# Kernel optimization log

Hardware: AMD Instinct MI355X
Metric: run time of the kernel (lower is better)

## Reference

```python
import jax, jax.numpy as jnp
import numpy as np

B, T, D_MODEL, N_HEAD = 8, 1024, 1024, 8
D_K = D_MODEL // N_HEAD  # = d_v = 128; V projection shared across heads


def setup_inputs() -> dict:
    key = jax.random.key(0)
    ks = jax.random.split(key, 8)
    scale = 0.02
    q = jax.random.normal(ks[0], (B, T, D_MODEL), jnp.float32)
    k = jax.random.normal(ks[1], (B, T, D_MODEL), jnp.float32)
    v = jax.random.normal(ks[2], (B, T, D_MODEL), jnp.float32)
    # causal mask, 1.0 = attend, broadcast to batch (shape (B, T, T))
    mask = jnp.broadcast_to(jnp.tril(jnp.ones((T, T), jnp.float32)), (B, T, T))
    Wq = jax.random.normal(ks[3], (N_HEAD, D_MODEL, D_K), jnp.float32) * scale
    Wk = jax.random.normal(ks[4], (N_HEAD, D_MODEL, D_K), jnp.float32) * scale
    Wv = jax.random.normal(ks[5], (D_MODEL, D_K), jnp.float32) * scale  # shared across heads
    Wo = jax.random.normal(ks[6], (D_K, D_MODEL), jnp.float32) * scale
    return {"q": q, "k": k, "v": v, "mask": mask, "Wq": Wq, "Wk": Wk, "Wv": Wv, "Wo": Wo}


def reference(q, k, v, mask, Wq, Wk, Wv, Wo):
    # Per-head Q/K projections (batched over heads), shared V projection.
    qh = jnp.einsum('btd,hdk->hbtk', q, Wq)  # (H,B,T,d_k)
    kh = jnp.einsum('bsd,hdk->hbsk', k, Wk)  # (H,B,S,d_k)
    vh = jnp.einsum('bsd,dk->bsk', v, Wv)    # (B,S,d_v) shared across heads
    temper = jnp.sqrt(jnp.asarray(qh.shape[-1], jnp.float32))
    scores = jnp.einsum('hbtk,hbsk->hbts', qh, kh) / temper
    scores = scores + (-1e9) * (1.0 - mask)[None]  # additive mask per head
    attn = jax.nn.softmax(scores, axis=-1)          # (H,B,T,S)
    heads = jnp.einsum('hbts,bsk->hbtk', attn, vh)  # (H,B,T,d_v)
    out = jnp.einsum('btk,kd->btd', heads.mean(axis=0), Wo)  # mean over heads, then w_o
    return out, attn  # dropout rate 0.0 / inference -> identity
```

## Files before the change

kernel.cpp:

```cpp
#include <hip/hip_runtime.h>
#include <cstdint>

typedef __attribute__((ext_vector_type(8))) short bf16x8;
typedef __attribute__((ext_vector_type(4))) float f32x4;

constexpr int NH = 8, NB = 8, SEQ = 1024, DM = 1024, DK = 128;
constexpr int MTOT = NB * SEQ;

__device__ __forceinline__ unsigned short f2bf(float f) {
    unsigned int u = __float_as_uint(f);
    unsigned int r = (u + 0x7fffu + ((u >> 16) & 1u)) >> 16;
    return (unsigned short)r;
}
__device__ __forceinline__ float bf2f(unsigned int s) {
    return __uint_as_float((s & 0xffffu) << 16);
}
__device__ __forceinline__ void gld16(const void* g, void* l) {
    __builtin_amdgcn_global_load_lds((const __attribute__((address_space(1))) void*)g,
                                     (__attribute__((address_space(3))) void*)l, 16, 0, 0);
}
__device__ __forceinline__ int ti_of_slot(int v) {
    int u = v & 3, s2 = v >> 2;
    return (s2 == 0) ? u : (s2 == 1) ? (15 - u) : (s2 == 2) ? (8 + u) : (7 - u);
}

__global__ __launch_bounds__(256) void transpose_w_kernel(
    const float* __restrict__ Wq, const float* __restrict__ Wk,
    const float* __restrict__ Wv, const float* __restrict__ Wo,
    unsigned short* __restrict__ WqT, unsigned short* __restrict__ WkT,
    unsigned short* __restrict__ WvT, unsigned short* __restrict__ WoT)
{
    const int s = blockIdx.y;
    const float* in; unsigned short* out; int R, C;
    if (s < 8)        { in = Wq + (size_t)s * DM * DK;       out = WqT + (size_t)s * DK * DM;       R = DM; C = DK; }
    else if (s < 16)  { in = Wk + (size_t)(s - 8) * DM * DK; out = WkT + (size_t)(s - 8) * DK * DM; R = DM; C = DK; }
    else if (s == 16) { in = Wv; out = WvT; R = DM; C = DK; }
    else              { in = Wo; out = WoT; R = DK; C = DM; }
    const int tc = C / 32;
    const int r0 = (blockIdx.x / tc) * 32, c0 = (blockIdx.x % tc) * 32;
    __shared__ unsigned short t[32][33];
    const int tid = threadIdx.x;
    const int a = tid >> 3, b4 = (tid & 7) * 4;
    float4 f = *reinterpret_cast<const float4*>(&in[(size_t)(r0 + a) * C + c0 + b4]);
    t[a][b4 + 0] = f2bf(f.x); t[a][b4 + 1] = f2bf(f.y);
    t[a][b4 + 2] = f2bf(f.z); t[a][b4 + 3] = f2bf(f.w);
    __syncthreads();
    ushort4 o;
    o.x = t[b4 + 0][a]; o.y = t[b4 + 1][a]; o.z = t[b4 + 2][a]; o.w = t[b4 + 3][a];
    *reinterpret_cast<ushort4*>(&out[(size_t)(c0 + a) * R + r0 + b4]) = o;
}

__global__ __launch_bounds__(256) void cvt_kernel(
    const float* __restrict__ q, const float* __restrict__ k, const float* __restrict__ v,
    unsigned short* __restrict__ qb, unsigned short* __restrict__ kb,
    unsigned short* __restrict__ vb)
{
    const float* src; unsigned short* dst;
    const int s = blockIdx.y;
    if (s == 0)      { src = q; dst = qb; }
    else if (s == 1) { src = k; dst = kb; }
    else             { src = v; dst = vb; }
    const size_t base = ((size_t)blockIdx.x * 256 + threadIdx.x) * 8;
    float4 f0 = *reinterpret_cast<const float4*>(&src[base]);
    float4 f1 = *reinterpret_cast<const float4*>(&src[base + 4]);
    uint4 o;
    o.x = (unsigned int)f2bf(f0.x) | ((unsigned int)f2bf(f0.y) << 16);
    o.y = (unsigned int)f2bf(f0.z) | ((unsigned int)f2bf(f0.w) << 16);
    o.z = (unsigned int)f2bf(f1.x) | ((unsigned int)f2bf(f1.y) << 16);
    o.w = (unsigned int)f2bf(f1.z) | ((unsigned int)f2bf(f1.w) << 16);
    *reinterpret_cast<uint4*>(&dst[base]) = o;
}

__global__ __launch_bounds__(256) void proj_kernel(
    const unsigned short* __restrict__ qb, const unsigned short* __restrict__ kb,
    const unsigned short* __restrict__ vb,
    const unsigned short* __restrict__ WqT, const unsigned short* __restrict__ WkT,
    const unsigned short* __restrict__ WvT,
    unsigned short* __restrict__ qh, unsigned short* __restrict__ kh,
    unsigned short* __restrict__ vt)
{
    const int g = blockIdx.x, m0 = blockIdx.y * 128;
    const unsigned short* Ab; const unsigned short* Bt;
    if (g < 8)       { Ab = qb; Bt = WqT + (size_t)g * DK * DM; }
    else if (g < 16) { Ab = kb; Bt = WkT + (size_t)(g - 8) * DK * DM; }
    else             { Ab = vb; Bt = WvT; }

    __shared__ unsigned short As[2][128][32];
    __shared__ unsigned short Bs[2][128][32];

    const int tid = threadIdx.x, wave = tid >> 6, lane = tid & 63, quad = lane >> 4, l15 = lane & 15;
    const int wm = (wave & 1) * 64, wn = (wave >> 1) * 64;

    f32x4 acc[4][4];
    for (int mi = 0; mi < 4; ++mi)
        for (int ni = 0; ni < 4; ++ni)
            acc[mi][ni] = (f32x4){0.f, 0.f, 0.f, 0.f};

    const int s_row = tid >> 2;
    const int s_col = ((tid & 3) ^ ((s_row >> 1) & 3)) * 8;
    const unsigned short* gA = Ab + (size_t)(m0 + s_row) * DM + s_col;
    const unsigned short* gAh = Ab + (size_t)(m0 + 64 + s_row) * DM + s_col;
    const unsigned short* gB = Bt + (size_t)s_row * DM + s_col;
    const unsigned short* gBh = Bt + (size_t)(64 + s_row) * DM + s_col;
    char* lA = (char*)&As[0][0][0] + wave * 1024;
    char* lB = (char*)&Bs[0][0][0] + wave * 1024;
    const int rcb = (quad ^ ((l15 >> 1) & 3)) * 8;

    auto STAGE = [&](int k0, int bsel) {
        gld16(gA + k0, lA + bsel * 8192);
        gld16(gAh + k0, lA + bsel * 8192 + 4096);
        gld16(gB + k0, lB + bsel * 8192);
        gld16(gBh + k0, lB + bsel * 8192 + 4096);
    };

    int bsel = 0;
    STAGE(0, 0);
    __syncthreads();
    for (int k0 = 0; k0 < DM; k0 += 32) {
        if (k0 + 32 < DM) STAGE(k0 + 32, bsel ^ 1);
        bf16x8 af[4], bfr[4];
        for (int mi = 0; mi < 4; ++mi)
            af[mi] = *reinterpret_cast<const bf16x8*>(&As[bsel][wm + mi * 16 + l15][rcb]);
        for (int ni = 0; ni < 4; ++ni)
            bfr[ni] = *reinterpret_cast<const bf16x8*>(&Bs[bsel][wn + ni * 16 + l15][rcb]);
        for (int mi = 0; mi < 4; ++mi)
            for (int ni = 0; ni < 4; ++ni)
                acc[mi][ni] = __builtin_amdgcn_mfma_f32_16x16x32_bf16(af[mi], bfr[ni], acc[mi][ni], 0, 0, 0);
        __syncthreads();
        bsel ^= 1;
    }

    if (g < 16) {
        unsigned short* C = (g < 8) ? (qh + (size_t)g * MTOT * DK)
                                    : (kh + (size_t)(g - 8) * MTOT * DK);
        for (int mi = 0; mi < 4; ++mi)
            for (int ni = 0; ni < 4; ++ni)
                for (int r = 0; r < 4; ++r)
                    C[(size_t)(m0 + wm + mi * 16 + quad * 4 + r) * DK + wn + ni * 16 + l15] =
                        f2bf(acc[mi][ni][r]);
    } else {
        for (int mi = 0; mi < 4; ++mi)
            for (int ni = 0; ni < 4; ++ni)
                for (int r = 0; r < 4; ++r) {
                    int row = m0 + wm + mi * 16 + quad * 4 + r;
                    int col = wn + ni * 16 + l15;
                    vt[((size_t)(row >> 10) * DK + col) * SEQ + (row & 1023)] = f2bf(acc[mi][ni][r]);
                }
    }
}

__global__ __launch_bounds__(256) void attn_lse_kernel(
    const unsigned short* __restrict__ qh, const unsigned short* __restrict__ kh,
    float* __restrict__ linv)
{
    const int hb = blockIdx.x;
    const int ti = ti_of_slot(blockIdx.y);

    const unsigned short* kbase = kh + (size_t)hb * SEQ * DK;
    const unsigned short* qbase = qh + ((size_t)hb * SEQ + ti * 64) * DK;

    __shared__ unsigned short Ks[2][4][64][32];

    const int tid = threadIdx.x, wave = tid >> 6, lane = tid & 63, quad = lane >> 4, l15 = lane & 15;
    const float scale = 0.08838834764831843f;

    int koff[4]; char* kdst[4];
#pragma unroll
    for (int i = 0; i < 4; ++i) {
        int slot = wave * 256 + i * 64 + lane;
        int ks = slot >> 8, row = (slot >> 2) & 63;
        int c = (slot & 3) ^ ((row >> 1) & 3);
        koff[i] = row * DK + ks * 32 + c * 8;
        kdst[i] = (char*)&Ks[0][0][0][0] + slot * 16;
    }
    auto STAGE = [&](int j, int bsel) {
        const unsigned short* src = kbase + (size_t)j * 64 * DK;
#pragma unroll
        for (int i = 0; i < 4; ++i) gld16(src + koff[i], kdst[i] + bsel * 16384);
    };

    const int rcb = (quad ^ ((l15 >> 1) & 3)) * 8;

    bf16x8 aq[4];
    for (int ks = 0; ks < 4; ++ks)
        aq[ks] = *reinterpret_cast<const bf16x8*>(
            &qbase[(size_t)(wave * 16 + l15) * DK + ks * 32 + quad * 8]);

    const int trow_base = ti * 64 + wave * 16 + quad * 4;
    float l_run[4] = {0.f, 0.f, 0.f, 0.f};

    int bsel = 0;
    STAGE(0, 0);
    __syncthreads();
    for (int j = 0; j <= ti; ++j) {
        if (j < ti) STAGE(j + 1, bsel ^ 1);
        f32x4 sacc[4];
        for (int ni = 0; ni < 4; ++ni) sacc[ni] = (f32x4){0.f, 0.f, 0.f, 0.f};
        for (int ks = 0; ks < 4; ++ks)
            for (int ni = 0; ni < 4; ++ni) {
                bf16x8 bb = *reinterpret_cast<const bf16x8*>(&Ks[bsel][ks][ni * 16 + l15][rcb]);
                sacc[ni] = __builtin_amdgcn_mfma_f32_16x16x32_bf16(aq[ks], bb, sacc[ni], 0, 0, 0);
            }
        const bool diag = (j == ti);
        for (int r = 0; r < 4; ++r) {
            float lsum = 0.f;
            for (int ni = 0; ni < 4; ++ni) {
                int s = j * 64 + ni * 16 + l15;
                float e = __expf(sacc[ni][r] * scale);
                lsum += (!diag || s <= trow_base + r) ? e : 0.f;
            }
            for (int off = 1; off < 16; off <<= 1)
                lsum += __shfl_xor(lsum, off, 64);
            l_run[r] += lsum;
        }
        __syncthreads();
        bsel ^= 1;
    }

    if (l15 == 0)
        for (int r = 0; r < 4; ++r)
            linv[(size_t)hb * SEQ + ti * 64 + wave * 16 + quad * 4 + r] = 1.f / l_run[r];
}

__global__ __launch_bounds__(256) void attn_pv_kernel(
    const unsigned short* __restrict__ qh, const unsigned short* __restrict__ kh,
    const unsigned short* __restrict__ vt, const float* __restrict__ linv,
    unsigned short* __restrict__ heads, float* __restrict__ attn)
{
    const int hb = blockIdx.x, b = hb & 7;
    const int ti = ti_of_slot(blockIdx.y);

    const unsigned short* kbase = kh + (size_t)hb * SEQ * DK;
    const unsigned short* vbase = vt + (size_t)b * DK * SEQ;
    const unsigned short* qbase = qh + ((size_t)hb * SEQ + ti * 64) * DK;
    float* attn_base            = attn + ((size_t)hb * SEQ + ti * 64) * SEQ;
    unsigned short* hbase       = heads + ((size_t)hb * SEQ + ti * 64) * DK;

    __shared__ unsigned short Ks[2][4][64][32];
    __shared__ unsigned short Vs[2][128][64];
    __shared__ unsigned short Ps[64][72];

    const int tid = threadIdx.x, wave = tid >> 6, lane = tid & 63, quad = lane >> 4, l15 = lane & 15;
    const float scale = 0.08838834764831843f;

    int koff[4]; char* kdst[4]; int voff[4]; char* vdst[4];
#pragma unroll
    for (int i = 0; i < 4; ++i) {
        int slot = wave * 256 + i * 64 + lane;
        {
            int ks = slot >> 8, row = (slot >> 2) & 63;
            int c = (slot & 3) ^ ((row >> 1) & 3);
            koff[i] = row * DK + ks * 32 + c * 8;
            kdst[i] = (char*)&Ks[0][0][0][0] + slot * 16;
        }
        {
            int row = slot >> 3;
            int c = (slot & 7) ^ (row & 7);
            voff[i] = row * SEQ + c * 8;
            vdst[i] = (char*)&Vs[0][0][0] + slot * 16;
        }
    }
    auto STAGE = [&](int j, int bsel) {
        const unsigned short* srcK = kbase + (size_t)j * 64 * DK;
        const unsigned short* srcV = vbase + j * 64;
#pragma unroll
        for (int i = 0; i < 4; ++i) {
            gld16(srcK + koff[i], kdst[i] + bsel * 16384);
            gld16(srcV + voff[i], vdst[i] + bsel * 16384);
        }
    };

    const int rcb = (quad ^ ((l15 >> 1) & 3)) * 8;
    const int vxor = l15 & 7;

    bf16x8 aq[4];
    for (int ks = 0; ks < 4; ++ks)
        aq[ks] = *reinterpret_cast<const bf16x8*>(
            &qbase[(size_t)(wave * 16 + l15) * DK + ks * 32 + quad * 8]);

    float inv_l[4];
    for (int r = 0; r < 4; ++r)
        inv_l[r] = linv[(size_t)hb * SEQ + ti * 64 + wave * 16 + quad * 4 + r];

    const int trow_base = ti * 64 + wave * 16 + quad * 4;
    f32x4 oacc[8];
    for (int n = 0; n < 8; ++n) oacc[n] = (f32x4){0.f, 0.f, 0.f, 0.f};

    int bsel = 0;
    STAGE(0, 0);
    __syncthreads();
    for (int j = 0; j <= ti; ++j) {
        if (j < ti) STAGE(j + 1, bsel ^ 1);
        f32x4 sacc[4];
        for (int ni = 0; ni < 4; ++ni) sacc[ni] = (f32x4){0.f, 0.f, 0.f, 0.f};
        for (int ks = 0; ks < 4; ++ks)
            for (int ni = 0; ni < 4; ++ni) {
                bf16x8 bb = *reinterpret_cast<const bf16x8*>(&Ks[bsel][ks][ni * 16 + l15][rcb]);
                sacc[ni] = __builtin_amdgcn_mfma_f32_16x16x32_bf16(aq[ks], bb, sacc[ni], 0, 0, 0);
            }
        const bool diag = (j == ti);
        for (int r = 0; r < 4; ++r)
            for (int ni = 0; ni < 4; ++ni) {
                int s = j * 64 + ni * 16 + l15;
                float pv = (!diag || s <= trow_base + r)
                              ? __expf(sacc[ni][r] * scale) * inv_l[r] : 0.f;
                __builtin_nontemporal_store(
                    pv, &attn_base[(size_t)(wave * 16 + quad * 4 + r) * SEQ + s]);
                Ps[wave * 16 + quad * 4 + r][ni * 16 + l15] = f2bf(pv);
            }
        for (int ks2 = 0; ks2 < 2; ++ks2) {
            bf16x8 ap = *reinterpret_cast<const bf16x8*>(&Ps[wave * 16 + l15][ks2 * 32 + quad * 8]);
            const int c = (ks2 * 4 + quad) ^ vxor;
            for (int n2 = 0; n2 < 8; ++n2) {
                bf16x8 bv = *reinterpret_cast<const bf16x8*>(&Vs[bsel][n2 * 16 + l15][c * 8]);
                oacc[n2] = __builtin_amdgcn_mfma_f32_16x16x32_bf16(ap, bv, oacc[n2], 0, 0, 0);
            }
        }
        __syncthreads();
        bsel ^= 1;
    }

    for (int n2 = 0; n2 < 8; ++n2)
        for (int r = 0; r < 4; ++r)
            hbase[(size_t)(wave * 16 + quad * 4 + r) * DK + n2 * 16 + l15] = f2bf(oacc[n2][r]);

    {
        const int s0 = (ti + 1) * 64;
        if (s0 < SEQ) {
            const int z4 = (SEQ - s0) >> 2;
            f32x4 zz = {0.f, 0.f, 0.f, 0.f};
            for (int r = 0; r < 64; ++r)
                for (int c = tid; c < z4; c += 256)
                    __builtin_nontemporal_store(zz, (f32x4*)&attn_base[(size_t)r * SEQ + s0 + c * 4]);
        }
    }
}

__global__ __launch_bounds__(256) void mean_kernel(
    const unsigned short* __restrict__ heads, unsigned short* __restrict__ hmean)
{
    size_t base = ((size_t)blockIdx.x * 256 + threadIdx.x) * 8;
    float s[8] = {0.f, 0.f, 0.f, 0.f, 0.f, 0.f, 0.f, 0.f};
    for (int h = 0; h < 8; ++h) {
        uint4 u = *reinterpret_cast<const uint4*>(&heads[(size_t)h * MTOT * DK + base]);
        s[0] += bf2f(u.x); s[1] += bf2f(u.x >> 16);
        s[2] += bf2f(u.y); s[3] += bf2f(u.y >> 16);
        s[4] += bf2f(u.z); s[5] += bf2f(u.z >> 16);
        s[6] += bf2f(u.w); s[7] += bf2f(u.w >> 16);
    }
    uint4 o;
    o.x = (unsigned int)f2bf(s[0] * 0.125f) | ((unsigned int)f2bf(s[1] * 0.125f) << 16);
    o.y = (unsigned int)f2bf(s[2] * 0.125f) | ((unsigned int)f2bf(s[3] * 0.125f) << 16);
    o.z = (unsigned int)f2bf(s[4] * 0.125f) | ((unsigned int)f2bf(s[5] * 0.125f) << 16);
    o.w = (unsigned int)f2bf(s[6] * 0.125f) | ((unsigned int)f2bf(s[7] * 0.125f) << 16);
    *reinterpret_cast<uint4*>(&hmean[base]) = o;
}

__global__ __launch_bounds__(256) void out_kernel(
    const unsigned short* __restrict__ hmean, const unsigned short* __restrict__ WoT,
    float* __restrict__ out)
{
    const int n0 = blockIdx.x * 128, m0 = blockIdx.y * 128;
    __shared__ unsigned short As[128][32];
    __shared__ unsigned short Bs[128][32];

    const int tid = threadIdx.x, wave = tid >> 6, lane = tid & 63, quad = lane >> 4, l15 = lane & 15;
    const int wm = (wave & 1) * 64, wn = (wave >> 1) * 64;

    f32x4 acc[4][4];
    for (int mi = 0; mi < 4; ++mi)
        for (int ni = 0; ni < 4; ++ni)
            acc[mi][ni] = (f32x4){0.f, 0.f, 0.f, 0.f};

    const unsigned short* gA0 = hmean + (size_t)(m0 + (tid >> 2)) * DK + (tid & 3) * 8;
    const unsigned short* gB0 = WoT + (size_t)(n0 + (tid >> 2)) * DK + (tid & 3) * 8;
    char* lA = (char*)&As[0][0] + wave * 1024;
    char* lB = (char*)&Bs[0][0] + wave * 1024;

    for (int k0 = 0; k0 < DK; k0 += 32) {
        __syncthreads();
        gld16(gA0 + k0, lA); gld16(gA0 + k0 + 64 * DK, lA + 4096);
        gld16(gB0 + k0, lB); gld16(gB0 + k0 + 64 * DK, lB + 4096);
        __syncthreads();
        bf16x8 af[4], bfr[4];
        for (int mi = 0; mi < 4; ++mi)
            af[mi] = *reinterpret_cast<const bf16x8*>(&As[wm + mi * 16 + l15][quad * 8]);
        for (int ni = 0; ni < 4; ++ni)
            bfr[ni] = *reinterpret_cast<const bf16x8*>(&Bs[wn + ni * 16 + l15][quad * 8]);
        for (int mi = 0; mi < 4; ++mi)
            for (int ni = 0; ni < 4; ++ni)
                acc[mi][ni] = __builtin_amdgcn_mfma_f32_16x16x32_bf16(af[mi], bfr[ni], acc[mi][ni], 0, 0, 0);
    }
    for (int mi = 0; mi < 4; ++mi)
        for (int ni = 0; ni < 4; ++ni)
            for (int r = 0; r < 4; ++r)
                out[(size_t)(m0 + wm + mi * 16 + quad * 4 + r) * DM + n0 + wn + ni * 16 + l15] =
                    acc[mi][ni][r];
}

extern "C" void kernel_launch(void* const* d_in, const int* in_sizes, int n_in,
                              void* d_out, int out_size, void* d_ws, size_t ws_size,
                              hipStream_t stream) {
    (void)in_sizes; (void)n_in; (void)out_size; (void)ws_size;
    const float* q  = (const float*)d_in[0];
    const float* k  = (const float*)d_in[1];
    const float* v  = (const float*)d_in[2];
    const float* Wq = (const float*)d_in[4];
    const float* Wk = (const float*)d_in[5];
    const float* Wv = (const float*)d_in[6];
    const float* Wo = (const float*)d_in[7];

    float* out  = (float*)d_out;
    float* attn = out + (size_t)NB * SEQ * DM;
    unsigned short* heads = (unsigned short*)d_out;
    unsigned short* qb = (unsigned short*)attn;
    unsigned short* kb = qb + (size_t)MTOT * DM;
    unsigned short* vb = kb + (size_t)MTOT * DM;

    unsigned short* ws    = (unsigned short*)d_ws;
    unsigned short* WqT   = ws;
    unsigned short* WkT   = WqT + (size_t)NH * DK * DM;
    unsigned short* WvT   = WkT + (size_t)NH * DK * DM;
    unsigned short* WoT   = WvT + (size_t)DK * DM;
    unsigned short* qh    = WoT + (size_t)DM * DK;
    unsigned short* kh    = qh + (size_t)NH * MTOT * DK;
    unsigned short* vt    = kh + (size_t)NH * MTOT * DK;
    unsigned short* hmean = vt + (size_t)NB * DK * SEQ;
    float* linv           = (float*)(hmean + (size_t)MTOT * DK);

    transpose_w_kernel<<<dim3(128, 18), 256, 0, stream>>>(Wq, Wk, Wv, Wo, WqT, WkT, WvT, WoT);
    cvt_kernel<<<dim3(4096, 3), 256, 0, stream>>>(q, k, v, qb, kb, vb);
    proj_kernel<<<dim3(17, 64), 256, 0, stream>>>(qb, kb, vb, WqT, WkT, WvT, qh, kh, vt);
    attn_lse_kernel<<<dim3(64, 16), 256, 0, stream>>>(qh, kh, linv);
    attn_pv_kernel<<<dim3(64, 16), 256, 0, stream>>>(qh, kh, vt, linv, heads, attn);
    mean_kernel<<<512, 256, 0, stream>>>(heads, hmean);
    out_kernel<<<dim3(8, 64), 256, 0, stream>>>(hmean, WoT, out);
}
```

Measured before the change: 569.3 us.

## Deepen projection GEMM pipeline and replace syncthreads with fine-grained vmcnt waits

The projection GEMM moves from a double buffer to a four-slot LDS ring with two tiles in flight. Each step waits on a partial vmcnt count and a raw s_barrier instead of a full __syncthreads drain. The two attention kernels use the same split: barrier, issue the next stage, wait partial vmcnt, barrier. The aim is to overlap global-to-LDS loads with MFMA work rather than draining all memory ops every iteration. This relies on the hand-counted vmcnt values matching the outstanding loads, and doubles the GEMM's LDS use, which can lower occupancy. In the PV kernel the nontemporal attn stores also count against vmcnt, which could make the waits stricter than intended.

```diff
diff --git a/kernel.cpp b/kernel.cpp
--- a/kernel.cpp
+++ b/kernel.cpp
@@ -85,8 +85,8 @@
     else if (g < 16) { Ab = kb; Bt = WkT + (size_t)(g - 8) * DK * DM; }
     else             { Ab = vb; Bt = WvT; }
 
-    __shared__ unsigned short As[2][128][32];
-    __shared__ unsigned short Bs[2][128][32];
+    __shared__ unsigned short As[4][128][32];
+    __shared__ unsigned short Bs[4][128][32];
 
     const int tid = threadIdx.x, wave = tid >> 6, lane = tid & 63, quad = lane >> 4, l15 = lane & 15;
     const int wm = (wave & 1) * 64, wn = (wave >> 1) * 64;
@@ -106,28 +106,34 @@
     char* lB = (char*)&Bs[0][0][0] + wave * 1024;
     const int rcb = (quad ^ ((l15 >> 1) & 3)) * 8;
 
-    auto STAGE = [&](int k0, int bsel) {
-        gld16(gA + k0, lA + bsel * 8192);
-        gld16(gAh + k0, lA + bsel * 8192 + 4096);
-        gld16(gB + k0, lB + bsel * 8192);
-        gld16(gBh + k0, lB + bsel * 8192 + 4096);
+    auto STAGE = [&](int kt, int buf) {
+        gld16(gA + kt * 32, lA + buf * 8192);
+        gld16(gAh + kt * 32, lA + buf * 8192 + 4096);
+        gld16(gB + kt * 32, lB + buf * 8192);
+        gld16(gBh + kt * 32, lB + buf * 8192 + 4096);
     };
 
-    int bsel = 0;
     STAGE(0, 0);
-    __syncthreads();
-    for (int k0 = 0; k0 < DM; k0 += 32) {
-        if (k0 + 32 < DM) STAGE(k0 + 32, bsel ^ 1);
+    STAGE(1, 1);
+    for (int t = 0; t < 32; ++t) {
+        if (t + 2 < 32) {
+            STAGE(t + 2, (t + 2) & 3);
+            asm volatile("s_waitcnt vmcnt(8)" ::: "memory");
+        } else if (t + 1 < 32) {
+            asm volatile("s_waitcnt vmcnt(4)" ::: "memory");
+        } else {
+            asm volatile("s_waitcnt vmcnt(0)" ::: "memory");
+        }
+        __builtin_amdgcn_s_barrier();
+        const int bs = t & 3;
         bf16x8 af[4], bfr[4];
         for (int mi = 0; mi < 4; ++mi)
-            af[mi] = *reinterpret_cast<const bf16x8*>(&As[bsel][wm + mi * 16 + l15][rcb]);
+            af[mi] = *reinterpret_cast<const bf16x8*>(&As[bs][wm + mi * 16 + l15][rcb]);
         for (int ni = 0; ni < 4; ++ni)
-            bfr[ni] = *reinterpret_cast<const bf16x8*>(&Bs[bsel][wn + ni * 16 + l15][rcb]);
+            bfr[ni] = *reinterpret_cast<const bf16x8*>(&Bs[bs][wn + ni * 16 + l15][rcb]);
         for (int mi = 0; mi < 4; ++mi)
             for (int ni = 0; ni < 4; ++ni)
                 acc[mi][ni] = __builtin_amdgcn_mfma_f32_16x16x32_bf16(af[mi], bfr[ni], acc[mi][ni], 0, 0, 0);
-        __syncthreads();
-        bsel ^= 1;
     }
 
     if (g < 16) {
@@ -189,11 +195,17 @@
     const int trow_base = ti * 64 + wave * 16 + quad * 4;
     float l_run[4] = {0.f, 0.f, 0.f, 0.f};
 
-    int bsel = 0;
     STAGE(0, 0);
-    __syncthreads();
     for (int j = 0; j <= ti; ++j) {
-        if (j < ti) STAGE(j + 1, bsel ^ 1);
+        __builtin_amdgcn_s_barrier();
+        if (j < ti) {
+            STAGE(j + 1, (j + 1) & 1);
+            asm volatile("s_waitcnt vmcnt(4)" ::: "memory");
+        } else {
+            asm volatile("s_waitcnt vmcnt(0)" ::: "memory");
+        }
+        __builtin_amdgcn_s_barrier();
+        const int bsel = j & 1;
         f32x4 sacc[4];
         for (int ni = 0; ni < 4; ++ni) sacc[ni] = (f32x4){0.f, 0.f, 0.f, 0.f};
         for (int ks = 0; ks < 4; ++ks)
@@ -213,8 +225,6 @@
                 lsum += __shfl_xor(lsum, off, 64);
             l_run[r] += lsum;
         }
-        __syncthreads();
-        bsel ^= 1;
     }
 
     if (l15 == 0)
@@ -286,11 +296,17 @@
     f32x4 oacc[8];
     for (int n = 0; n < 8; ++n) oacc[n] = (f32x4){0.f, 0.f, 0.f, 0.f};
 
-    int bsel = 0;
     STAGE(0, 0);
-    __syncthreads();
     for (int j = 0; j <= ti; ++j) {
-        if (j < ti) STAGE(j + 1, bsel ^ 1);
+        __builtin_amdgcn_s_barrier();
+        if (j < ti) {
+            STAGE(j + 1, (j + 1) & 1);
+            asm volatile("s_waitcnt vmcnt(8)" ::: "memory");
+        } else {
+            asm volatile("s_waitcnt vmcnt(0)" ::: "memory");
+        }
+        __builtin_amdgcn_s_barrier();
+        const int bsel = j & 1;
         f32x4 sacc[4];
         for (int ni = 0; ni < 4; ++ni) sacc[ni] = (f32x4){0.f, 0.f, 0.f, 0.f};
         for (int ks = 0; ks < 4; ++ks)
@@ -316,8 +332,6 @@
                 oacc[n2] = __builtin_amdgcn_mfma_f32_16x16x32_bf16(ap, bv, oacc[n2], 0, 0, 0);
             }
         }
-        __syncthreads();
-        bsel ^= 1;
     }
 
     for (int n2 = 0; n2 < 8; ++n2)
```

New measurement: 531.1 us. -6.7%, faster.
